# Performance work log

Hardware: AMD Instinct MI355X
Metric: run time of the kernel (lower is better)

Reference implementation:

```python
import jax, jax.numpy as jnp
import numpy as np

# ---- fixed hyperparameters from init_kwargs / module defaults ----
ALPHA = 5.0      # SLAYER surrogate sharpness
C = 0.4          # SLAYER surrogate scale
THR = 1.0
ADAPT_COEFF = 1.0
DT = 1.0
B, T, IN, OUT = 64, 1000, 512, 512


def setup_inputs() -> dict:
    key = jax.random.key(0)
    k = jax.random.split(key, 6)
    x = jax.random.normal(k[0], (B, T, IN), dtype=jnp.float32)
    lim = 1.0 / np.sqrt(IN)
    weight = jax.random.uniform(k[1], (OUT, IN), jnp.float32, -lim, lim)
    bias = jnp.zeros((OUT,), jnp.float32)
    # orthogonal recurrent init (gain 1.0)
    recurrent, _ = jnp.linalg.qr(jax.random.normal(k[2], (OUT, OUT), jnp.float32))
    beta = jax.random.uniform(k[3], (OUT,), jnp.float32, 0.0, 1.0)
    beta2 = jax.random.uniform(k[4], (OUT,), jnp.float32, 0.0, 2.0)
    # fixed tau trainers: decay = exp(-dt / tau)
    decay_v = jnp.full((OUT,), np.exp(-DT / 20.0), jnp.float32)          # tau_soma = 20
    tau_adapt = jax.random.uniform(k[5], (OUT,), jnp.float32, 20.0, 200.0)
    decay_b = jnp.exp(-DT / tau_adapt)
    return {"input_tensor": x, "weight": weight, "bias": bias,
            "recurrent": recurrent, "beta": beta, "beta2": beta2,
            "decay_v": decay_v, "decay_b": decay_b}


def _spike(v_thr):
    # forward value: heaviside(v_thr, 1.0); gradient: SLAYER surrogate
    sg = jax.lax.stop_gradient
    heavi = sg(jnp.where(v_thr >= 0, 1.0, 0.0).astype(v_thr.dtype))
    surr = sg(C * ALPHA / (2.0 * jnp.exp(jnp.abs(v_thr) * ALPHA)))
    return heavi + (v_thr - sg(v_thr)) * surr


def _alif_forward(input_tensor, weight, bias, recurrent, beta, beta2, decay_v, decay_b):
    b_sz = input_tensor.shape[0]
    out_f = weight.shape[0]
    z0 = jnp.zeros((b_sz, out_f), input_tensor.dtype)
    # precompute feedforward soma currents for all timesteps: [T, B, OUT]
    cur_in = jnp.einsum('bti,oi->tbo', input_tensor, weight) + bias

    def step(carry, c_t):
        v, z, b = carry
        v = v * (1.0 - z)                          # reset to zero on spike
        cur = c_t + z @ recurrent.T                # recurrent current
        v_t = decay_v * v + (1.0 - decay_v) * (cur - b)
        z_t = _spike(v_t - THR)
        b_t = decay_b * b + (1.0 - decay_b) * (beta * v_t + beta2 * z_t) * ADAPT_COEFF
        return (v_t, z_t, b_t), (v_t, z_t, b_t)

    _, (vs, zs, bs) = jax.lax.scan(step, (z0, z0, z0), cur_in)
    # [T,B,O] -> [B,T,O]
    vs, zs, bs = (jnp.swapaxes(a, 0, 1) for a in (vs, zs, bs))
    pad = z0[:, None, :]                            # initial state at t=0
    v_full = jnp.concatenate([pad, vs], axis=1)
    z_full = jnp.concatenate([pad, zs], axis=1)
    b_full = jnp.concatenate([pad, bs], axis=1)
    states = jnp.stack([v_full, z_full, b_full], axis=0)  # [3, B, T+1, O]
    return zs, states


def reference(input_tensor, weight, bias, recurrent, beta, beta2, decay_v, decay_b):
    return _alif_forward(input_tensor, weight, bias, recurrent, beta, beta2, decay_v, decay_b)
```

## Files before the change

kernel.cpp:

```cpp
#include <hip/hip_runtime.h>
#include <stdint.h>

#define GB   64
#define GT   1000
#define GIN  512
#define GOUT 512
#define GM   (GB*GT)
#define NCH  20
#define CHL  50

typedef __attribute__((ext_vector_type(8))) __bf16 bf8_t;
typedef __attribute__((ext_vector_type(4))) float f4_t;
typedef __attribute__((ext_vector_type(8))) unsigned short us8_t;

typedef __attribute__((address_space(1))) const uint32_t gu32_t;
typedef __attribute__((address_space(3))) uint32_t lu32_t;

static __device__ __forceinline__ unsigned short f2bf(float f) {
    union { float f; unsigned u; } v; v.f = f;
    unsigned r = v.u + 0x7fffu + ((v.u >> 16) & 1u);
    return (unsigned short)(r >> 16);
}

#define NX8 4096000
#define NW8 32768
__global__ __launch_bounds__(256) void alif_cvt(
    const float* __restrict__ X, const float* __restrict__ W,
    unsigned short* __restrict__ Xh, unsigned short* __restrict__ Wh)
{
    const size_t i = (size_t)blockIdx.x * 256 + threadIdx.x;
    const float* src; unsigned short* dst;
    if (i < NX8) { src = X + i * 8; dst = Xh + i * 8; }
    else         { const size_t j = i - NX8; src = W + j * 8; dst = Wh + j * 8; }
    const float4 a = ((const float4*)src)[0];
    const float4 b = ((const float4*)src)[1];
    us8_t r;
    r[0] = f2bf(a.x); r[1] = f2bf(a.y); r[2] = f2bf(a.z); r[3] = f2bf(a.w);
    r[4] = f2bf(b.x); r[5] = f2bf(b.y); r[6] = f2bf(b.z); r[7] = f2bf(b.w);
    *(us8_t*)dst = r;
}

__global__ __launch_bounds__(256) void alif_gemm(
    const unsigned short* __restrict__ Xh, const unsigned short* __restrict__ Wh,
    const float* __restrict__ bias, float* __restrict__ cur)
{
    __shared__ unsigned short As[128 * 32];
    __shared__ unsigned short Bs[128 * 32];
    const int tid  = threadIdx.x;
    const int bn   = blockIdx.x & 3;
    const int bm   = blockIdx.x >> 2;
    const int lane = tid & 63;
    const int wave = tid >> 6;
    const int wm   = (wave >> 1) * 64;
    const int wn   = (wave & 1) * 64;
    const int quad = lane >> 4;
    const int l15  = lane & 15;
    const int srow = lane >> 2;
    const int scol = (lane & 3) * 8;

    f4_t acc[4][4];
    #pragma unroll
    for (int i = 0; i < 4; ++i)
        #pragma unroll
        for (int j = 0; j < 4; ++j) acc[i][j] = (f4_t)(0.0f);

    for (int k0 = 0; k0 < GIN; k0 += 32) {
        #pragma unroll
        for (int s = wave; s < 8; s += 4) {
            const int row = s * 16 + srow;
            const unsigned short* ga = Xh + (size_t)(bm * 128 + row) * GIN + k0 + scol;
            const unsigned short* gb = Wh + (size_t)(bn * 128 + row) * GIN + k0 + scol;
            __builtin_amdgcn_global_load_lds((gu32_t*)ga, (lu32_t*)&As[s * 512], 16, 0, 0);
            __builtin_amdgcn_global_load_lds((gu32_t*)gb, (lu32_t*)&Bs[s * 512], 16, 0, 0);
        }
        __syncthreads();
        bf8_t afr[4], bfr[4];
        #pragma unroll
        for (int i = 0; i < 4; ++i) {
            afr[i] = *(const bf8_t*)(&As[(wm + i * 16 + l15) * 32 + quad * 8]);
            bfr[i] = *(const bf8_t*)(&Bs[(wn + i * 16 + l15) * 32 + quad * 8]);
        }
        #pragma unroll
        for (int i = 0; i < 4; ++i)
            #pragma unroll
            for (int j = 0; j < 4; ++j)
                acc[i][j] = __builtin_amdgcn_mfma_f32_16x16x32_bf16(afr[i], bfr[j], acc[i][j], 0, 0, 0);
        __syncthreads();
    }

    #pragma unroll
    for (int j = 0; j < 4; ++j) {
        const int col  = bn * 128 + wn + j * 16 + l15;
        const float bc = bias[col];
        #pragma unroll
        for (int i = 0; i < 4; ++i) {
            const int rowb = bm * 128 + wm + i * 16 + quad * 4;
            #pragma unroll
            for (int r = 0; r < 4; ++r)
                cur[(size_t)(rowb + r) * GOUT + col] = acc[i][j][r] + bc;
        }
    }
}

static __device__ __forceinline__ void alif_mat(
    float dv, float db, float be,
    float& a00, float& a01, float& a10, float& a11, float& g0, float& g1)
{
    a00 = dv;
    a01 = -(1.0f - dv);
    g0  = (1.0f - dv);
    a10 = (1.0f - db) * be * dv;
    a11 = db - (1.0f - db) * be * (1.0f - dv);
    g1  = (1.0f - db) * be * (1.0f - dv);
}

__global__ __launch_bounds__(256) void alif_pass1(
    const float* __restrict__ out,
    const float* __restrict__ beta, const float* __restrict__ decay_v,
    const float* __restrict__ decay_b, float2* __restrict__ u)
{
    const int gid = blockIdx.x * 256 + threadIdx.x;
    const int o = gid & (GOUT - 1);
    const int r = gid >> 9;
    const int c = r % NCH;
    const int b = r / NCH;
    float a00, a01, a10, a11, g0, g1;
    alif_mat(decay_v[o], decay_b[o], beta[o], a00, a01, a10, a11, g0, g1);

    const float* cp = out + ((size_t)b * GT + c * CHL) * GOUT + o;
    float v = 0.f, w = 0.f;
    float buf[10];
    #pragma unroll
    for (int j = 0; j < 10; ++j) buf[j] = cp[(size_t)j * GOUT];
    for (int t0 = 0; t0 < CHL; t0 += 10) {
        float nxt[10];
        const bool more = (t0 + 10 < CHL);
        if (more) {
            #pragma unroll
            for (int j = 0; j < 10; ++j) nxt[j] = cp[(size_t)(t0 + 10 + j) * GOUT];
        }
        #pragma unroll
        for (int j = 0; j < 10; ++j) {
            const float cu = buf[j];
            const float nv = a00 * v + a01 * w + g0 * cu;
            const float nw = a10 * v + a11 * w + g1 * cu;
            v = nv; w = nw;
        }
        if (more) {
            #pragma unroll
            for (int j = 0; j < 10; ++j) buf[j] = nxt[j];
        }
    }
    u[((size_t)b * NCH + c) * GOUT + o] = make_float2(v, w);
}

__global__ __launch_bounds__(256) void alif_pass2(
    float2* __restrict__ u,
    const float* __restrict__ beta, const float* __restrict__ decay_v,
    const float* __restrict__ decay_b)
{
    const int gid = blockIdx.x * 256 + threadIdx.x;
    const int o = gid & (GOUT - 1);
    const int b = gid >> 9;
    float a00, a01, a10, a11, g0, g1;
    alif_mat(decay_v[o], decay_b[o], beta[o], a00, a01, a10, a11, g0, g1);
    float p00 = 1.f, p01 = 0.f, p10 = 0.f, p11 = 1.f;
    for (int i = 0; i < CHL; ++i) {
        const float n00 = a00 * p00 + a01 * p10, n01 = a00 * p01 + a01 * p11;
        const float n10 = a10 * p00 + a11 * p10, n11 = a10 * p01 + a11 * p11;
        p00 = n00; p01 = n01; p10 = n10; p11 = n11;
    }
    float Sv = 0.f, Sb = 0.f;
    for (int c = 0; c < NCH; ++c) {
        const size_t idx = ((size_t)b * NCH + c) * GOUT + o;
        const float2 t = u[idx];
        u[idx] = make_float2(Sv, Sb);
        const float nSv = p00 * Sv + p01 * Sb + t.x;
        const float nSb = p10 * Sv + p11 * Sb + t.y;
        Sv = nSv; Sb = nSb;
    }
}

__global__ __launch_bounds__(256) void alif_pass3(
    float* __restrict__ out, const float2* __restrict__ seed,
    const float* __restrict__ beta, const float* __restrict__ beta2,
    const float* __restrict__ decay_v, const float* __restrict__ decay_b,
    unsigned int* __restrict__ flag)
{
    const int gid = blockIdx.x * 256 + threadIdx.x;
    const int o = gid & (GOUT - 1);
    const int r = gid >> 9;
    const int c = r % NCH;
    const int b = r / NCH;
    const float dv = decay_v[o], db = decay_b[o];
    const float be = beta[o],    be2 = beta2[o];

    const int tbase = c * CHL;
    float* curp = out + ((size_t)b * GT + tbase) * GOUT + o;
    const size_t SB = (size_t)GB * GT * GOUT;
    const size_t PL = (size_t)GB * (GT + 1) * GOUT;
    float* vf  = out + SB + ((size_t)b * (GT + 1) + tbase + 1) * GOUT + o;
    float* zf  = vf + PL;
    float* bfp = vf + 2 * PL;
    if (c == 0) {
        vf[-(ptrdiff_t)GOUT] = 0.f; zf[-(ptrdiff_t)GOUT] = 0.f; bfp[-(ptrdiff_t)GOUT] = 0.f;
    }

    const float2 s0 = seed[((size_t)b * NCH + c) * GOUT + o];
    float v = s0.x, ba = s0.y, z = 0.f;
    bool any = false;
    float buf[10];
    #pragma unroll
    for (int j = 0; j < 10; ++j) buf[j] = curp[(size_t)j * GOUT];

    for (int t0 = 0; t0 < CHL; t0 += 10) {
        float nxt[10];
        const bool more = (t0 + 10 < CHL);
        if (more) {
            #pragma unroll
            for (int j = 0; j < 10; ++j) nxt[j] = curp[(size_t)(t0 + 10 + j) * GOUT];
        }
        #pragma unroll
        for (int j = 0; j < 10; ++j) {
            const int t = t0 + j;
            v *= (1.0f - z);
            v = dv * v + (1.0f - dv) * (buf[j] - ba);
            z = (v >= 1.0f) ? 1.0f : 0.0f;
            ba = db * ba + (1.0f - db) * (be * v + be2 * z);
            any = any || (z != 0.0f);
            curp[(size_t)t * GOUT]     = z;
            vf[(size_t)t * GOUT]       = v;
            zf[(size_t)t * GOUT]       = z;
            bfp[(size_t)t * GOUT]      = ba;
        }
        if (more) {
            #pragma unroll
            for (int j = 0; j < 10; ++j) buf[j] = nxt[j];
        }
    }
    if (any) atomicOr(flag, 1u);
}

__global__ __launch_bounds__(128) void alif_scan(
    float* __restrict__ out,
    const float* __restrict__ beta, const float* __restrict__ beta2,
    const float* __restrict__ decay_v, const float* __restrict__ decay_b,
    unsigned int* __restrict__ flag)
{
    const int gid = blockIdx.x * 128 + threadIdx.x;
    const int o = gid & (GOUT - 1);
    const int b = gid >> 9;
    const float dv = decay_v[o], db = decay_b[o];
    const float be = beta[o],    be2 = beta2[o];
    float* curp = out + (size_t)b * GT * GOUT + o;
    const size_t SB = (size_t)GB * GT * GOUT;
    const size_t PL = (size_t)GB * (GT + 1) * GOUT;
    float* vf  = out + SB + (size_t)b * (GT + 1) * GOUT + o;
    float* zf  = vf + PL;
    float* bfp = vf + 2 * PL;
    vf[0] = 0.f; zf[0] = 0.f; bfp[0] = 0.f;
    float v = 0.f, z = 0.f, ba = 0.f;
    bool any = false;
    float buf[8];
    #pragma unroll
    for (int j = 0; j < 8; ++j) buf[j] = curp[(size_t)j * GOUT];
    for (int t0 = 0; t0 < GT; t0 += 8) {
        float nxt[8];
        const bool more = (t0 + 8 < GT);
        if (more) {
            #pragma unroll
            for (int j = 0; j < 8; ++j) nxt[j] = curp[(size_t)(t0 + 8 + j) * GOUT];
        }
        #pragma unroll
        for (int j = 0; j < 8; ++j) {
            const int t = t0 + j;
            v *= (1.0f - z);
            v = dv * v + (1.0f - dv) * (buf[j] - ba);
            z = (v >= 1.0f) ? 1.0f : 0.0f;
            ba = db * ba + (1.0f - db) * (be * v + be2 * z);
            any = any || (z != 0.0f);
            curp[(size_t)t * GOUT]      = z;
            vf[(size_t)(t + 1) * GOUT]  = v;
            zf[(size_t)(t + 1) * GOUT]  = z;
            bfp[(size_t)(t + 1) * GOUT] = ba;
        }
        if (more) {
            #pragma unroll
            for (int j = 0; j < 8; ++j) buf[j] = nxt[j];
        }
    }
    if (any) atomicOr(flag, 1u);
}

__global__ __launch_bounds__(512) void alif_exact(
    const float* __restrict__ X, const float* __restrict__ W,
    const float* __restrict__ bias, const float* __restrict__ R,
    const float* __restrict__ beta, const float* __restrict__ beta2,
    const float* __restrict__ decay_v, const float* __restrict__ decay_b,
    float* __restrict__ out, const unsigned int* __restrict__ flag)
{
    if (*flag == 0u) return;
    const int b = blockIdx.x;
    const int o = threadIdx.x;
    __shared__ float xs[GIN];
    __shared__ float zsh[GOUT];
    __shared__ int sflag;
    const float dv = decay_v[o], db = decay_b[o];
    const float be = beta[o],    be2 = beta2[o];
    const float bi = bias[o];
    float* zsp = out + (size_t)b * GT * GOUT + o;
    const size_t SB = (size_t)GB * GT * GOUT, PL = (size_t)GB * (GT + 1) * GOUT;
    float* vf  = out + SB + (size_t)b * (GT + 1) * GOUT + o;
    float* zf  = vf + PL;
    float* bfp = vf + 2 * PL;
    vf[0] = 0.f; zf[0] = 0.f; bfp[0] = 0.f;
    float v = 0.f, z = 0.f, ba = 0.f;
    const float* wr = W + (size_t)o * GIN;
    const float* rr = R + (size_t)o * GOUT;
    for (int t = 0; t < GT; ++t) {
        __syncthreads();
        xs[o]  = X[((size_t)b * GT + t) * GIN + o];
        zsh[o] = z;
        if (o == 0) sflag = 0;
        __syncthreads();
        if (z != 0.f) sflag = 1;
        __syncthreads();
        float cur = bi;
        #pragma unroll 8
        for (int i = 0; i < GIN; ++i) cur += wr[i] * xs[i];
        if (sflag) {
            #pragma unroll 8
            for (int i = 0; i < GOUT; ++i) cur += rr[i] * zsh[i];
        }
        v *= (1.f - z);
        v = dv * v + (1.f - dv) * (cur - ba);
        z = (v >= 1.f) ? 1.f : 0.f;
        ba = db * ba + (1.f - db) * (be * v + be2 * z);
        zsp[(size_t)t * GOUT]       = z;
        vf[(size_t)(t + 1) * GOUT]  = v;
        zf[(size_t)(t + 1) * GOUT]  = z;
        bfp[(size_t)(t + 1) * GOUT] = ba;
    }
}

extern "C" void kernel_launch(void* const* d_in, const int* in_sizes, int n_in,
                              void* d_out, int out_size, void* d_ws, size_t ws_size,
                              hipStream_t stream)
{
    const float* X     = (const float*)d_in[0];
    const float* W     = (const float*)d_in[1];
    const float* bias  = (const float*)d_in[2];
    const float* R     = (const float*)d_in[3];
    const float* beta  = (const float*)d_in[4];
    const float* beta2 = (const float*)d_in[5];
    const float* dv    = (const float*)d_in[6];
    const float* db    = (const float*)d_in[7];
    float* out = (float*)d_out;
    unsigned int* flag = (unsigned int*)d_ws;

    const size_t SB = (size_t)GB * GT * GOUT;
    unsigned short* Xh = (unsigned short*)(out + SB);
    unsigned short* Wh = Xh + (size_t)GM * GIN;

    hipMemsetAsync(flag, 0, sizeof(unsigned int), stream);
    alif_cvt<<<dim3((NX8 + NW8) / 256), dim3(256), 0, stream>>>(X, W, Xh, Wh);
    alif_gemm<<<dim3(500 * 4), dim3(256), 0, stream>>>(Xh, Wh, bias, out);

    const size_t need = 256 + (size_t)GB * NCH * GOUT * sizeof(float2);
    if (ws_size >= need) {
        float2* u = (float2*)((char*)d_ws + 256);
        alif_pass1<<<dim3(GB * NCH * GOUT / 256), dim3(256), 0, stream>>>(out, beta, dv, db, u);
        alif_pass2<<<dim3(GB * GOUT / 256), dim3(256), 0, stream>>>(u, beta, dv, db);
        alif_pass3<<<dim3(GB * NCH * GOUT / 256), dim3(256), 0, stream>>>(out, u, beta, beta2, dv, db, flag);
    } else {
        alif_scan<<<dim3(256), dim3(128), 0, stream>>>(out, beta, beta2, dv, db, flag);
    }
    alif_exact<<<dim3(GB), dim3(512), 0, stream>>>(X, W, bias, R, beta, beta2, dv, db, out, flag);
}
```

Measured before the change: 737.6 us.

## Store GEMM currents as fp16 in workspace and process two neurons per thread

The GEMM now writes the feedforward currents in fp16 to a workspace buffer instead of fp32. The pass1 and pass3 scan kernels read that buffer and each thread handles two neurons with vectorized loads and nontemporal stores. The flag reset moves into the convert kernel in place of a separate memset, and the convert kernel uses nontemporal loads. This halves the memory traffic for the currents, but fp16 rounding can flip spikes near threshold. The exact-correction kernel may catch such cases, but it relies on the flag.

```diff
diff --git a/kernel.cpp b/kernel.cpp
--- a/kernel.cpp
+++ b/kernel.cpp
@@ -12,6 +12,8 @@
 typedef __attribute__((ext_vector_type(8))) __bf16 bf8_t;
 typedef __attribute__((ext_vector_type(4))) float f4_t;
 typedef __attribute__((ext_vector_type(8))) unsigned short us8_t;
+typedef __attribute__((ext_vector_type(2))) float f2v;
+typedef __attribute__((ext_vector_type(4))) float f4v;
 
 typedef __attribute__((address_space(1))) const uint32_t gu32_t;
 typedef __attribute__((address_space(3))) uint32_t lu32_t;
@@ -22,27 +24,51 @@
     return (unsigned short)(r >> 16);
 }
 
+static __device__ __forceinline__ unsigned short f2h(float f) {
+    _Float16 h = (_Float16)f;
+    unsigned short s; __builtin_memcpy(&s, &h, 2);
+    return s;
+}
+static __device__ __forceinline__ float lo_h(uint32_t u) {
+    unsigned short s = (unsigned short)(u & 0xffffu);
+    _Float16 h; __builtin_memcpy(&h, &s, 2);
+    return (float)h;
+}
+static __device__ __forceinline__ float hi_h(uint32_t u) {
+    unsigned short s = (unsigned short)(u >> 16);
+    _Float16 h; __builtin_memcpy(&h, &s, 2);
+    return (float)h;
+}
+static __device__ __forceinline__ void nts2(float* p, float x, float y) {
+    f2v v = {x, y};
+    __builtin_nontemporal_store(v, (f2v*)p);
+}
+
 #define NX8 4096000
 #define NW8 32768
 __global__ __launch_bounds__(256) void alif_cvt(
     const float* __restrict__ X, const float* __restrict__ W,
-    unsigned short* __restrict__ Xh, unsigned short* __restrict__ Wh)
-{
+    unsigned short* __restrict__ Xh, unsigned short* __restrict__ Wh,
+    unsigned int* __restrict__ flag)
+{
+    if (blockIdx.x == 0 && threadIdx.x == 0) *flag = 0u;
     const size_t i = (size_t)blockIdx.x * 256 + threadIdx.x;
     const float* src; unsigned short* dst;
     if (i < NX8) { src = X + i * 8; dst = Xh + i * 8; }
     else         { const size_t j = i - NX8; src = W + j * 8; dst = Wh + j * 8; }
-    const float4 a = ((const float4*)src)[0];
-    const float4 b = ((const float4*)src)[1];
+    const f4v a = __builtin_nontemporal_load((const f4v*)src);
+    const f4v b = __builtin_nontemporal_load((const f4v*)src + 1);
     us8_t r;
     r[0] = f2bf(a.x); r[1] = f2bf(a.y); r[2] = f2bf(a.z); r[3] = f2bf(a.w);
     r[4] = f2bf(b.x); r[5] = f2bf(b.y); r[6] = f2bf(b.z); r[7] = f2bf(b.w);
     *(us8_t*)dst = r;
 }
 
+template<bool HALF>
 __global__ __launch_bounds__(256) void alif_gemm(
     const unsigned short* __restrict__ Xh, const unsigned short* __restrict__ Wh,
-    const float* __restrict__ bias, float* __restrict__ cur)
+    const float* __restrict__ bias, float* __restrict__ cur,
+    unsigned short* __restrict__ curh)
 {
     __shared__ unsigned short As[128 * 32];
     __shared__ unsigned short Bs[128 * 32];
@@ -88,16 +114,23 @@
         __syncthreads();
     }
 
-    #pragma unroll
-    for (int j = 0; j < 4; ++j) {
-        const int col  = bn * 128 + wn + j * 16 + l15;
-        const float bc = bias[col];
-        #pragma unroll
-        for (int i = 0; i < 4; ++i) {
-            const int rowb = bm * 128 + wm + i * 16 + quad * 4;
-            #pragma unroll
-            for (int r = 0; r < 4; ++r)
-                cur[(size_t)(rowb + r) * GOUT + col] = acc[i][j][r] + bc;
+    float bcs[4];
+    #pragma unroll
+    for (int j = 0; j < 4; ++j) bcs[j] = bias[bn * 128 + wn + j * 16 + l15];
+    #pragma unroll
+    for (int i = 0; i < 4; ++i) {
+        const int rowb = bm * 128 + wm + i * 16 + quad * 4;
+        #pragma unroll
+        for (int r = 0; r < 4; ++r) {
+            #pragma unroll
+            for (int j = 0; j < 4; ++j) {
+                const int col  = bn * 128 + wn + j * 16 + l15;
+                const float v  = acc[i][j][r] + bcs[j];
+                if constexpr (HALF)
+                    curh[(size_t)(rowb + r) * GOUT + col] = f2h(v);
+                else
+                    cur[(size_t)(rowb + r) * GOUT + col] = v;
+            }
         }
     }
 }
@@ -112,6 +145,57 @@
     a10 = (1.0f - db) * be * dv;
     a11 = db - (1.0f - db) * be * (1.0f - dv);
     g1  = (1.0f - db) * be * (1.0f - dv);
+}
+
+__global__ __launch_bounds__(256) void alif_pass1_h(
+    const unsigned short* __restrict__ curh,
+    const float* __restrict__ beta, const float* __restrict__ decay_v,
+    const float* __restrict__ decay_b, float2* __restrict__ u)
+{
+    const int gid = blockIdx.x * 256 + threadIdx.x;
+    const int o2  = gid & 255;
+    const int o   = o2 * 2;
+    const int r   = gid >> 8;
+    const int c   = r % NCH;
+    const int b   = r / NCH;
+    const float2 dv2 = ((const float2*)decay_v)[o2];
+    const float2 db2 = ((const float2*)decay_b)[o2];
+    const float2 be2 = ((const float2*)beta)[o2];
+    float a00, a01, a10, a11, g0, g1;
+    float A00, A01, A10, A11, G0, G1;
+    alif_mat(dv2.x, db2.x, be2.x, a00, a01, a10, a11, g0, g1);
+    alif_mat(dv2.y, db2.y, be2.y, A00, A01, A10, A11, G0, G1);
+
+    const uint32_t* cp = (const uint32_t*)(curh + ((size_t)b * GT + (size_t)c * CHL) * GOUT + o);
+    float v0 = 0.f, w0 = 0.f, v1 = 0.f, w1 = 0.f;
+    uint32_t buf[10];
+    #pragma unroll
+    for (int j = 0; j < 10; ++j) buf[j] = cp[(size_t)j * 256];
+    for (int t0 = 0; t0 < CHL; t0 += 10) {
+        uint32_t nxt[10];
+        const bool more = (t0 + 10 < CHL);
+        if (more) {
+            #pragma unroll
+            for (int j = 0; j < 10; ++j) nxt[j] = cp[(size_t)(t0 + 10 + j) * 256];
+        }
+        #pragma unroll
+        for (int j = 0; j < 10; ++j) {
+            const float c0 = lo_h(buf[j]);
+            const float c1 = hi_h(buf[j]);
+            float nv = a00 * v0 + a01 * w0 + g0 * c0;
+            float nw = a10 * v0 + a11 * w0 + g1 * c0;
+            v0 = nv; w0 = nw;
+            nv = A00 * v1 + A01 * w1 + G0 * c1;
+            nw = A10 * v1 + A11 * w1 + G1 * c1;
+            v1 = nv; w1 = nw;
+        }
+        if (more) {
+            #pragma unroll
+            for (int j = 0; j < 10; ++j) buf[j] = nxt[j];
+        }
+    }
+    f4v s = {v0, w0, v1, w1};
+    *(f4v*)(u + ((size_t)b * NCH + c) * GOUT + o) = s;
 }
 
 __global__ __launch_bounds__(256) void alif_pass1(
@@ -179,6 +263,80 @@
         const float nSb = p10 * Sv + p11 * Sb + t.y;
         Sv = nSv; Sb = nSb;
     }
+}
+
+__global__ __launch_bounds__(256) void alif_pass3_h(
+    const unsigned short* __restrict__ curh, float* __restrict__ out,
+    const float2* __restrict__ seed,
+    const float* __restrict__ beta, const float* __restrict__ beta2,
+    const float* __restrict__ decay_v, const float* __restrict__ decay_b,
+    unsigned int* __restrict__ flag)
+{
+    const int gid = blockIdx.x * 256 + threadIdx.x;
+    const int o2  = gid & 255;
+    const int o   = o2 * 2;
+    const int r   = gid >> 8;
+    const int c   = r % NCH;
+    const int b   = r / NCH;
+    const float2 dv2 = ((const float2*)decay_v)[o2];
+    const float2 db2 = ((const float2*)decay_b)[o2];
+    const float2 be_ = ((const float2*)beta)[o2];
+    const float2 b2_ = ((const float2*)beta2)[o2];
+
+    const int tbase = c * CHL;
+    const uint32_t* cp = (const uint32_t*)(curh + ((size_t)b * GT + tbase) * GOUT + o);
+    float* zsp = out + ((size_t)b * GT + tbase) * GOUT + o;
+    const size_t SB = (size_t)GB * GT * GOUT;
+    const size_t PL = (size_t)GB * (GT + 1) * GOUT;
+    float* vf  = out + SB + ((size_t)b * (GT + 1) + tbase + 1) * GOUT + o;
+    float* zf  = vf + PL;
+    float* bfp = vf + 2 * PL;
+    if (c == 0) {
+        nts2(vf  - GOUT, 0.f, 0.f);
+        nts2(zf  - GOUT, 0.f, 0.f);
+        nts2(bfp - GOUT, 0.f, 0.f);
+    }
+
+    const f4v s0 = *(const f4v*)(seed + ((size_t)b * NCH + c) * GOUT + o);
+    float v0 = s0.x, ba0 = s0.y, v1 = s0.z, ba1 = s0.w;
+    float z0 = 0.f, z1 = 0.f;
+    bool any = false;
+    uint32_t buf[10];
+    #pragma unroll
+    for (int j = 0; j < 10; ++j) buf[j] = cp[(size_t)j * 256];
+
+    for (int t0 = 0; t0 < CHL; t0 += 10) {
+        uint32_t nxt[10];
+        const bool more = (t0 + 10 < CHL);
+        if (more) {
+            #pragma unroll
+            for (int j = 0; j < 10; ++j) nxt[j] = cp[(size_t)(t0 + 10 + j) * 256];
+        }
+        #pragma unroll
+        for (int j = 0; j < 10; ++j) {
+            const int t = t0 + j;
+            const float c0 = lo_h(buf[j]);
+            const float c1 = hi_h(buf[j]);
+            v0 *= (1.0f - z0);
+            v0 = dv2.x * v0 + (1.0f - dv2.x) * (c0 - ba0);
+            z0 = (v0 >= 1.0f) ? 1.0f : 0.0f;
+            ba0 = db2.x * ba0 + (1.0f - db2.x) * (be_.x * v0 + b2_.x * z0);
+            v1 *= (1.0f - z1);
+            v1 = dv2.y * v1 + (1.0f - dv2.y) * (c1 - ba1);
+            z1 = (v1 >= 1.0f) ? 1.0f : 0.0f;
+            ba1 = db2.y * ba1 + (1.0f - db2.y) * (be_.y * v1 + b2_.y * z1);
+            any = any || (z0 != 0.0f) || (z1 != 0.0f);
+            nts2(zsp + (size_t)t * GOUT, z0, z1);
+            nts2(vf  + (size_t)t * GOUT, v0, v1);
+            nts2(zf  + (size_t)t * GOUT, z0, z1);
+            nts2(bfp + (size_t)t * GOUT, ba0, ba1);
+        }
+        if (more) {
+            #pragma unroll
+            for (int j = 0; j < 10; ++j) buf[j] = nxt[j];
+        }
+    }
+    if (any) atomicOr(flag, 1u);
 }
 
 __global__ __launch_bounds__(256) void alif_pass3(
@@ -362,17 +520,27 @@
     unsigned short* Xh = (unsigned short*)(out + SB);
     unsigned short* Wh = Xh + (size_t)GM * GIN;
 
-    hipMemsetAsync(flag, 0, sizeof(unsigned int), stream);
-    alif_cvt<<<dim3((NX8 + NW8) / 256), dim3(256), 0, stream>>>(X, W, Xh, Wh);
-    alif_gemm<<<dim3(500 * 4), dim3(256), 0, stream>>>(Xh, Wh, bias, out);
-
-    const size_t need = 256 + (size_t)GB * NCH * GOUT * sizeof(float2);
-    if (ws_size >= need) {
+    const size_t seeds_b = (size_t)GB * NCH * GOUT * sizeof(float2);
+    const size_t need_f  = 256 + seeds_b;
+    const size_t need_h  = need_f + (size_t)GM * GOUT * 2;
+
+    alif_cvt<<<dim3((NX8 + NW8) / 256), dim3(256), 0, stream>>>(X, W, Xh, Wh, flag);
+
+    if (ws_size >= need_h) {
         float2* u = (float2*)((char*)d_ws + 256);
+        unsigned short* curh = (unsigned short*)((char*)d_ws + need_f);
+        alif_gemm<true><<<dim3(500 * 4), dim3(256), 0, stream>>>(Xh, Wh, bias, nullptr, curh);
+        alif_pass1_h<<<dim3(GB * NCH * GOUT / 512), dim3(256), 0, stream>>>(curh, beta, dv, db, u);
+        alif_pass2<<<dim3(GB * GOUT / 256), dim3(256), 0, stream>>>(u, beta, dv, db);
+        alif_pass3_h<<<dim3(GB * NCH * GOUT / 512), dim3(256), 0, stream>>>(curh, out, u, beta, beta2, dv, db, flag);
+    } else if (ws_size >= need_f) {
+        float2* u = (float2*)((char*)d_ws + 256);
+        alif_gemm<false><<<dim3(500 * 4), dim3(256), 0, stream>>>(Xh, Wh, bias, out, nullptr);
         alif_pass1<<<dim3(GB * NCH * GOUT / 256), dim3(256), 0, stream>>>(out, beta, dv, db, u);
         alif_pass2<<<dim3(GB * GOUT / 256), dim3(256), 0, stream>>>(u, beta, dv, db);
         alif_pass3<<<dim3(GB * NCH * GOUT / 256), dim3(256), 0, stream>>>(out, u, beta, beta2, dv, db, flag);
     } else {
+        alif_gemm<false><<<dim3(500 * 4), dim3(256), 0, stream>>>(Xh, Wh, bias, out, nullptr);
         alif_scan<<<dim3(256), dim3(128), 0, stream>>>(out, beta, beta2, dv, db, flag);
     }
     alif_exact<<<dim3(GB), dim3(512), 0, stream>>>(X, W, bias, R, beta, beta2, dv, db, out, flag);
```

New measurement: 688.4 us. 1.07x faster.
